# Optimization experiments

Hardware: AMD Instinct MI355X
Metric: run time of the kernel (lower is better)

## Reference

```python
import jax, jax.numpy as jnp
import numpy as np

BZ, SRC_LEN, TGT_LEN, DIM = 32, 1024, 1024, 512


def setup_inputs() -> dict:
    key = jax.random.key(0)
    k1, k2, k3, k4 = jax.random.split(key, 4)
    src = jax.random.normal(k1, (BZ, SRC_LEN, DIM), dtype=jnp.float32)
    tgt = jax.random.normal(k2, (BZ, TGT_LEN, DIM), dtype=jnp.float32)
    # lengths in [1, SRC_LEN] so every row has at least one valid position
    src_lengths = jax.random.randint(k3, (BZ,), 1, SRC_LEN + 1, dtype=jnp.int64)
    # nn.Linear(2*dim, dim, bias=False): weight shape (dim, 2*dim)
    bound = 1.0 / np.sqrt(2 * DIM)
    w_out = jax.random.uniform(k4, (DIM, 2 * DIM), dtype=jnp.float32,
                               minval=-bound, maxval=bound)
    return {"src": src, "tgt": tgt, "src_lengths": src_lengths, "w_out": w_out}


def reference(src, tgt, src_lengths, w_out):
    # dot-product attention scores: (bz, tgt_len, src_len)
    score = jnp.einsum("btd,bsd->bts", tgt, src)
    # mask out padded source positions (position >= length)
    valid = jnp.arange(src.shape[1])[None, :] < src_lengths[:, None]  # (bz, src_len)
    score = jnp.where(valid[:, None, :], score, -jnp.inf)
    align = jax.nn.softmax(score, axis=-1)
    # context: (bz, tgt_len, dim)
    c = jnp.einsum("bts,bsd->btd", align, src)
    concat_c = jnp.concatenate([c, tgt], axis=-1)  # (bz, tgt_len, 2*dim)
    attn_h = jnp.einsum("bte,de->btd", concat_c, w_out)
    return attn_h, align
```

## Files before the change

### kernel.cpp

```cpp
#include <hip/hip_runtime.h>
#include <hip/hip_bf16.h>

typedef __attribute__((ext_vector_type(4))) float  f32x4;
typedef __attribute__((ext_vector_type(4))) float  float4v;
typedef __attribute__((ext_vector_type(8))) short  bf16x8;
typedef __attribute__((ext_vector_type(4))) short  bf16x4;
typedef __attribute__((ext_vector_type(2))) unsigned int u32x2;

#define BZ   32
#define SLEN 1024
#define TLEN 1024
#define DIM  512
#define TILE 128
#define LP   40

#define PSEL 0x07060302u

__device__ __forceinline__ unsigned int fbits(float x) { return __builtin_bit_cast(unsigned int, x); }
__device__ __forceinline__ float fval(unsigned int u) { return __builtin_bit_cast(float, u); }

__device__ __forceinline__ unsigned short f2bf(float x) {
  unsigned int u = fbits(x);
  unsigned int r = u + 0x7FFFu + ((u >> 16) & 1u);
  return (unsigned short)(r >> 16);
}
__device__ __forceinline__ float bf2f(unsigned short h) { return fval(((unsigned int)h) << 16); }

__device__ __forceinline__ unsigned int packhi(float x0, float x1) {
  return __builtin_amdgcn_perm(fbits(x1), fbits(x0), PSEL);
}

__device__ __forceinline__ int get_len(const int* __restrict__ p, int b) {
  bool is64 = (p[1] == 0) && (p[3] == 0) && (p[5] == 0);
  return is64 ? p[2 * b] : p[b];
}

#define TLP 68
__global__ __launch_bounds__(256) void k_transpose(
    const float* __restrict__ src, unsigned short* __restrict__ srcT) {
  const int b  = blockIdx.z;
  const int s0 = blockIdx.x * 64;
  const int d0 = blockIdx.y * 64;
  __shared__ unsigned short tl[64 * TLP];
  const int tid = threadIdx.x;
#pragma unroll
  for (int r = 0; r < 4; ++r) {
    const int idx = tid + 256 * r;
    const int row = idx >> 4, c4 = idx & 15;
    float4v x = *(const float4v*)(src + ((size_t)(b * SLEN + s0 + row)) * DIM + d0 + c4 * 4);
    unsigned short* pp = tl + row * TLP + c4 * 4;
    pp[0] = f2bf(x[0]); pp[1] = f2bf(x[1]); pp[2] = f2bf(x[2]); pp[3] = f2bf(x[3]);
  }
  __syncthreads();
#pragma unroll
  for (int r = 0; r < 2; ++r) {
    const int idx  = tid + 256 * r;
    const int drow = idx >> 3, c8 = idx & 7;
    union { unsigned short u[8]; bf16x8 v; } pk;
#pragma unroll
    for (int j = 0; j < 8; ++j) pk.u[j] = tl[(c8 * 8 + j) * TLP + drow];
    *(bf16x8*)(srcT + ((size_t)(b * DIM + d0 + drow)) * SLEN + s0 + c8 * 8) = pk.v;
  }
}

__global__ __launch_bounds__(256) void k_prep_w(
    const float* __restrict__ w, unsigned short* __restrict__ wbf) {
  const size_t i = ((size_t)blockIdx.x * 256 + threadIdx.x) * 8;
  float4v x0 = *(const float4v*)(w + i);
  float4v x1 = *(const float4v*)(w + i + 4);
  union { unsigned short u[8]; bf16x8 v; } hi;
#pragma unroll
  for (int j = 0; j < 4; ++j) { hi.u[j] = f2bf(x0[j]); hi.u[4 + j] = f2bf(x1[j]); }
  *(bf16x8*)(wbf + i) = hi.v;
}

__global__ __launch_bounds__(256) void k_score(
    const float* __restrict__ tgt, const float* __restrict__ src,
    const int* __restrict__ lens, float* __restrict__ align_out) {
  const int j    = blockIdx.x;
  const int xcd  = j & 7;
  const int seq  = j >> 3;
  const int b    = ((seq >> 6) << 3) | xcd;
  const int tile = seq & 63;
  const int t0   = (tile >> 3) * TILE;
  const int s0   = (tile & 7) * TILE;
  const int len  = get_len(lens, b);
  if (s0 >= len) return;

  __shared__ short aHi[TILE * LP], aLo[TILE * LP], bHi[TILE * LP], bLo[TILE * LP];

  const int tid  = threadIdx.x;
  const int lane = tid & 63;
  const int wid  = tid >> 6;
  const int wt   = wid >> 1, wsd = wid & 1;
  const int g    = lane >> 4, r16 = lane & 15;
  const int srow = tid >> 3, sc4 = tid & 7;

  f32x4 acc[4][4];
#pragma unroll
  for (int m = 0; m < 4; ++m)
#pragma unroll
    for (int n = 0; n < 4; ++n) acc[m][n] = (f32x4){0.f, 0.f, 0.f, 0.f};

  const float* tgtB = tgt + ((size_t)(b * TLEN + t0)) * DIM;
  const float* srcB = src + ((size_t)(b * SLEN + s0)) * DIM;

  float4v va[4], vb[4];
#pragma unroll
  for (int r = 0; r < 4; ++r) {
    const int row = srow + 32 * r;
    va[r] = *(const float4v*)(tgtB + (size_t)row * DIM + sc4 * 4);
    vb[r] = *(const float4v*)(srcB + (size_t)row * DIM + sc4 * 4);
  }

  for (int k0 = 0; k0 < DIM; k0 += 32) {
#pragma unroll
    for (int r = 0; r < 4; ++r) {
      const int row = srow + 32 * r;
      u32x2 ah, al, bh, bl;
      ah[0] = packhi(va[r][0], va[r][1]); ah[1] = packhi(va[r][2], va[r][3]);
      bh[0] = packhi(vb[r][0], vb[r][1]); bh[1] = packhi(vb[r][2], vb[r][3]);
      float ra0 = va[r][0] - fval(fbits(va[r][0]) & 0xFFFF0000u);
      float ra1 = va[r][1] - fval(fbits(va[r][1]) & 0xFFFF0000u);
      float ra2 = va[r][2] - fval(fbits(va[r][2]) & 0xFFFF0000u);
      float ra3 = va[r][3] - fval(fbits(va[r][3]) & 0xFFFF0000u);
      float rb0 = vb[r][0] - fval(fbits(vb[r][0]) & 0xFFFF0000u);
      float rb1 = vb[r][1] - fval(fbits(vb[r][1]) & 0xFFFF0000u);
      float rb2 = vb[r][2] - fval(fbits(vb[r][2]) & 0xFFFF0000u);
      float rb3 = vb[r][3] - fval(fbits(vb[r][3]) & 0xFFFF0000u);
      al[0] = packhi(ra0, ra1); al[1] = packhi(ra2, ra3);
      bl[0] = packhi(rb0, rb1); bl[1] = packhi(rb2, rb3);
      const int o = row * LP + sc4 * 4;
      *(u32x2*)(aHi + o) = ah; *(u32x2*)(aLo + o) = al;
      *(u32x2*)(bHi + o) = bh; *(u32x2*)(bLo + o) = bl;
    }
    if (k0 + 32 < DIM) {
#pragma unroll
      for (int r = 0; r < 4; ++r) {
        const int row = srow + 32 * r;
        va[r] = *(const float4v*)(tgtB + (size_t)row * DIM + (k0 + 32) + sc4 * 4);
        vb[r] = *(const float4v*)(srcB + (size_t)row * DIM + (k0 + 32) + sc4 * 4);
      }
    }
    __syncthreads();
    bf16x8 fbh[4], fbl[4];
#pragma unroll
    for (int n = 0; n < 4; ++n) {
      const int row = wsd * 64 + n * 16 + r16;
      fbh[n] = *(const bf16x8*)(bHi + row * LP + g * 8);
      fbl[n] = *(const bf16x8*)(bLo + row * LP + g * 8);
    }
#pragma unroll
    for (int m = 0; m < 4; ++m) {
      const int row = wt * 64 + m * 16 + r16;
      bf16x8 fah = *(const bf16x8*)(aHi + row * LP + g * 8);
      bf16x8 fal = *(const bf16x8*)(aLo + row * LP + g * 8);
#pragma unroll
      for (int n = 0; n < 4; ++n) {
        acc[m][n] = __builtin_amdgcn_mfma_f32_16x16x32_bf16(fah, fbh[n], acc[m][n], 0, 0, 0);
        acc[m][n] = __builtin_amdgcn_mfma_f32_16x16x32_bf16(fal, fbh[n], acc[m][n], 0, 0, 0);
        acc[m][n] = __builtin_amdgcn_mfma_f32_16x16x32_bf16(fah, fbl[n], acc[m][n], 0, 0, 0);
      }
    }
    __syncthreads();
  }
  float* outB = align_out + ((size_t)(b * TLEN + t0)) * SLEN + s0;
#pragma unroll
  for (int m = 0; m < 4; ++m) {
    const int tr = wt * 64 + m * 16 + g * 4;
#pragma unroll
    for (int n = 0; n < 4; ++n) {
      const int sc = wsd * 64 + n * 16 + r16;
#pragma unroll
      for (int r = 0; r < 4; ++r)
        outB[(size_t)(tr + r) * SLEN + sc] = acc[m][n][r];
    }
  }
}

__global__ __launch_bounds__(256) void k_softmax(
    const int* __restrict__ lens, float* __restrict__ align_io) {
  const int row  = blockIdx.x * 4 + (threadIdx.x >> 6);
  const int lane = threadIdx.x & 63;
  const int b    = row >> 10;
  const int len  = get_len(lens, b);
  float* p = align_io + (size_t)row * SLEN;
  float v[4][4];
  float mx = -3.0e38f;
#pragma unroll
  for (int q = 0; q < 4; ++q) {
    if (256 * q >= len) {
#pragma unroll
      for (int j = 0; j < 4; ++j) v[q][j] = 0.f;
      continue;
    }
    const int sb = (lane + 64 * q) * 4;
    float4v x = *(const float4v*)(p + sb);
#pragma unroll
    for (int j = 0; j < 4; ++j) {
      v[q][j] = (sb + j < len) ? x[j] : 0.f;
      if (sb + j < len) mx = fmaxf(mx, x[j]);
    }
  }
#pragma unroll
  for (int off = 1; off < 64; off <<= 1) mx = fmaxf(mx, __shfl_xor(mx, off));
  float sum = 0.f;
#pragma unroll
  for (int q = 0; q < 4; ++q) {
    const int sb = (lane + 64 * q) * 4;
#pragma unroll
    for (int j = 0; j < 4; ++j) {
      float e = (sb + j < len) ? __expf(v[q][j] - mx) : 0.f;
      v[q][j] = e; sum += e;
    }
  }
#pragma unroll
  for (int off = 1; off < 64; off <<= 1) sum += __shfl_xor(sum, off);
  const float inv = 1.f / sum;
#pragma unroll
  for (int q = 0; q < 4; ++q) {
    float4v x;
#pragma unroll
    for (int j = 0; j < 4; ++j) x[j] = v[q][j] * inv;
    *(float4v*)(p + (lane + 64 * q) * 4) = x;
  }
}

__global__ __launch_bounds__(256) void k_pv(
    const float* __restrict__ align_in, const unsigned short* __restrict__ srcT,
    const int* __restrict__ lens, unsigned short* __restrict__ cws) {
  const int j    = blockIdx.x;
  const int xcd  = j & 7;
  const int seq  = j >> 3;
  const int b    = ((seq >> 5) << 3) | xcd;
  const int tile = seq & 31;
  const int t0   = (tile >> 2) * TILE;
  const int d0   = (tile & 3) * TILE;
  const int len = get_len(lens, b);
  const int ksteps = (len + 31) >> 5;

  __shared__ short A[TILE * LP], B[TILE * LP];
  const int tid  = threadIdx.x;
  const int lane = tid & 63;
  const int wid  = tid >> 6;
  const int wt   = wid >> 1, wsd = wid & 1;
  const int g    = lane >> 4, r16 = lane & 15;

  f32x4 acc[4][4];
#pragma unroll
  for (int m = 0; m < 4; ++m)
#pragma unroll
    for (int n = 0; n < 4; ++n) acc[m][n] = (f32x4){0.f, 0.f, 0.f, 0.f};

  const int arow = tid >> 3, ac4 = tid & 7;
  const int brow = tid >> 2, bc8 = tid & 3;

  float4v xa[4];
  bf16x8  xb[2];
#pragma unroll
  for (int r = 0; r < 4; ++r)
    xa[r] = *(const float4v*)(align_in + ((size_t)(b * TLEN + t0 + arow + 32 * r)) * SLEN + ac4 * 4);
#pragma unroll
  for (int r = 0; r < 2; ++r)
    xb[r] = *(const bf16x8*)(srcT + ((size_t)(b * DIM + d0 + brow + 64 * r)) * SLEN + bc8 * 8);

  for (int ks = 0; ks < ksteps; ++ks) {
#pragma unroll
    for (int r = 0; r < 4; ++r) {
      u32x2 h;
      h[0] = packhi(xa[r][0], xa[r][1]); h[1] = packhi(xa[r][2], xa[r][3]);
      *(u32x2*)(A + (arow + 32 * r) * LP + ac4 * 4) = h;
    }
#pragma unroll
    for (int r = 0; r < 2; ++r)
      *(bf16x8*)(B + (brow + 64 * r) * LP + bc8 * 8) = xb[r];
    if (ks + 1 < ksteps) {
      const int k0 = (ks + 1) * 32;
#pragma unroll
      for (int r = 0; r < 4; ++r)
        xa[r] = *(const float4v*)(align_in + ((size_t)(b * TLEN + t0 + arow + 32 * r)) * SLEN + k0 + ac4 * 4);
#pragma unroll
      for (int r = 0; r < 2; ++r)
        xb[r] = *(const bf16x8*)(srcT + ((size_t)(b * DIM + d0 + brow + 64 * r)) * SLEN + k0 + bc8 * 8);
    }
    __syncthreads();
    bf16x8 fb[4];
#pragma unroll
    for (int n = 0; n < 4; ++n) fb[n] = *(const bf16x8*)(B + (wsd * 64 + n * 16 + r16) * LP + g * 8);
#pragma unroll
    for (int m = 0; m < 4; ++m) {
      bf16x8 fa = *(const bf16x8*)(A + (wt * 64 + m * 16 + r16) * LP + g * 8);
#pragma unroll
      for (int n = 0; n < 4; ++n)
        acc[m][n] = __builtin_amdgcn_mfma_f32_16x16x32_bf16(fa, fb[n], acc[m][n], 0, 0, 0);
    }
    __syncthreads();
  }
#pragma unroll
  for (int m = 0; m < 4; ++m) {
    const int tr = wt * 64 + m * 16 + g * 4;
#pragma unroll
    for (int n = 0; n < 4; ++n) {
      const int dc = wsd * 64 + n * 16 + r16;
#pragma unroll
      for (int r = 0; r < 4; ++r)
        cws[((size_t)(b * TLEN + t0 + tr + r)) * DIM + d0 + dc] = f2bf(acc[m][n][r]);
    }
  }
}

__global__ __launch_bounds__(256) void k_proj(
    const unsigned short* __restrict__ cws, const float* __restrict__ tgt,
    const unsigned short* __restrict__ wbf, float* __restrict__ attn_out) {
  const int j    = blockIdx.x;
  const int xcd  = j & 7;
  const int seq  = j >> 3;
  const int b    = ((seq >> 5) << 3) | xcd;
  const int tile = seq & 31;
  const int t0   = (tile >> 2) * TILE;
  const int d0   = (tile & 3) * TILE;

  __shared__ short A[TILE * LP], B[TILE * LP];
  const int tid  = threadIdx.x;
  const int lane = tid & 63;
  const int wid  = tid >> 6;
  const int wt   = wid >> 1, wsd = wid & 1;
  const int g    = lane >> 4, r16 = lane & 15;

  f32x4 acc[4][4];
#pragma unroll
  for (int m = 0; m < 4; ++m)
#pragma unroll
    for (int n = 0; n < 4; ++n) acc[m][n] = (f32x4){0.f, 0.f, 0.f, 0.f};

  for (int k0 = 0; k0 < 2 * DIM; k0 += 32) {
    if (k0 < DIM) {
#pragma unroll
      for (int r = 0; r < 2; ++r) {
        const int row = (tid >> 2) + 64 * r, c8 = tid & 3;
        bf16x8 x = *(const bf16x8*)(cws + ((size_t)(b * TLEN + t0 + row)) * DIM + k0 + c8 * 8);
        *(bf16x8*)(A + row * LP + c8 * 8) = x;
      }
    } else {
#pragma unroll
      for (int r = 0; r < 4; ++r) {
        const int row = (tid >> 3) + 32 * r, c4 = tid & 7;
        float4v x = *(const float4v*)(tgt + ((size_t)(b * TLEN + t0 + row)) * DIM + (k0 - DIM) + c4 * 4);
        bf16x4 h;
#pragma unroll
        for (int j2 = 0; j2 < 4; ++j2) h[j2] = (short)f2bf(x[j2]);
        *(bf16x4*)(A + row * LP + c4 * 4) = h;
      }
    }
#pragma unroll
    for (int r = 0; r < 2; ++r) {
      const int row = (tid >> 2) + 64 * r, c8 = tid & 3;
      bf16x8 x = *(const bf16x8*)(wbf + ((size_t)(d0 + row)) * (2 * DIM) + k0 + c8 * 8);
      *(bf16x8*)(B + row * LP + c8 * 8) = x;
    }
    __syncthreads();
    bf16x8 fb[4];
#pragma unroll
    for (int n = 0; n < 4; ++n) fb[n] = *(const bf16x8*)(B + (wsd * 64 + n * 16 + r16) * LP + g * 8);
#pragma unroll
    for (int m = 0; m < 4; ++m) {
      bf16x8 fa = *(const bf16x8*)(A + (wt * 64 + m * 16 + r16) * LP + g * 8);
#pragma unroll
      for (int n = 0; n < 4; ++n)
        acc[m][n] = __builtin_amdgcn_mfma_f32_16x16x32_bf16(fa, fb[n], acc[m][n], 0, 0, 0);
    }
    __syncthreads();
  }
#pragma unroll
  for (int m = 0; m < 4; ++m) {
    const int tr = wt * 64 + m * 16 + g * 4;
#pragma unroll
    for (int n = 0; n < 4; ++n) {
      const int dc = wsd * 64 + n * 16 + r16;
#pragma unroll
      for (int r = 0; r < 4; ++r)
        attn_out[((size_t)(b * TLEN + t0 + tr + r)) * DIM + d0 + dc] = acc[m][n][r];
    }
  }
}

extern "C" void kernel_launch(void* const* d_in, const int* in_sizes, int n_in,
                              void* d_out, int out_size, void* d_ws, size_t ws_size,
                              hipStream_t stream) {
  const float* src   = (const float*)d_in[0];
  const float* tgt   = (const float*)d_in[1];
  const int*   lens  = (const int*)d_in[2];
  const float* w_out = (const float*)d_in[3];

  float* attn_out  = (float*)d_out;
  float* align_out = attn_out + (size_t)BZ * TLEN * DIM;

  const size_t NE = (size_t)BZ * SLEN * DIM;
  const size_t NW = (size_t)DIM * 2 * DIM;
  unsigned short* srcT = (unsigned short*)d_ws;
  unsigned short* cws  = srcT + NE;
  unsigned short* wbf  = cws + NE;

  k_transpose<<<dim3(16, 8, BZ), 256, 0, stream>>>(src, srcT);
  k_prep_w<<<dim3((unsigned)(NW / 8 / 256)), 256, 0, stream>>>(w_out, wbf);
  k_score<<<dim3(2048), 256, 0, stream>>>(tgt, src, lens, align_out);
  k_softmax<<<dim3(BZ * TLEN / 4), 256, 0, stream>>>(lens, align_out);
  k_pv<<<dim3(1024), 256, 0, stream>>>(align_out, srcT, lens, cws);
  k_proj<<<dim3(1024), 256, 0, stream>>>(cws, tgt, wbf, attn_out);
}
```

Measured before the change: 262.3 us.

## Precompute bf16 hi/lo splits and load score tiles via global_load_lds

The fp32-to-bf16 hi/lo split of src and tgt moves out of the score GEMM into prep kernels that write split copies to workspace. The score kernel then streams those copies straight into LDS with global_load_lds, without register staging or in-loop conversion. This removes the conversion ALU work and register pressure from the GEMM loop. In exchange it adds extra passes that write about four bf16 copies of the inputs, and it drops the LDS padding and the register prefetch of the next k-slice, which may cause bank conflicts and less overlap. The hi/lo split also changes from truncation to round-to-nearest.

Measured after the change: 300.2 us. +14.4%, slower.

```diff
diff --git a/kernel.cpp b/kernel.cpp
--- a/kernel.cpp
+++ b/kernel.cpp
@@ -30,26 +30,44 @@
   return __builtin_amdgcn_perm(fbits(x1), fbits(x0), PSEL);
 }
 
+__device__ __forceinline__ void gld16(const void* g, void* l) {
+  __builtin_amdgcn_global_load_lds(
+      (const __attribute__((address_space(1))) void*)g,
+      (__attribute__((address_space(3))) void*)l, 16, 0, 0);
+}
+
 __device__ __forceinline__ int get_len(const int* __restrict__ p, int b) {
   bool is64 = (p[1] == 0) && (p[3] == 0) && (p[5] == 0);
   return is64 ? p[2 * b] : p[b];
 }
 
 #define TLP 68
-__global__ __launch_bounds__(256) void k_transpose(
-    const float* __restrict__ src, unsigned short* __restrict__ srcT) {
+__global__ __launch_bounds__(256) void k_prep_src(
+    const float* __restrict__ src, unsigned short* __restrict__ srcT,
+    unsigned short* __restrict__ srcHi, unsigned short* __restrict__ srcLo) {
   const int b  = blockIdx.z;
   const int s0 = blockIdx.x * 64;
   const int d0 = blockIdx.y * 64;
   __shared__ unsigned short tl[64 * TLP];
   const int tid = threadIdx.x;
 #pragma unroll
-  for (int r = 0; r < 4; ++r) {
+  for (int r = 0; r < 2; ++r) {
     const int idx = tid + 256 * r;
-    const int row = idx >> 4, c4 = idx & 15;
-    float4v x = *(const float4v*)(src + ((size_t)(b * SLEN + s0 + row)) * DIM + d0 + c4 * 4);
-    unsigned short* pp = tl + row * TLP + c4 * 4;
-    pp[0] = f2bf(x[0]); pp[1] = f2bf(x[1]); pp[2] = f2bf(x[2]); pp[3] = f2bf(x[3]);
+    const int row = idx >> 3, c8 = idx & 7;
+    const size_t goff = ((size_t)(b * SLEN + s0 + row)) * DIM + d0 + c8 * 8;
+    float4v x0 = *(const float4v*)(src + goff);
+    float4v x1 = *(const float4v*)(src + goff + 4);
+    union { unsigned short u[8]; bf16x8 v; } hi, lo;
+#pragma unroll
+    for (int j = 0; j < 4; ++j) {
+      unsigned short h0 = f2bf(x0[j]);
+      hi.u[j] = h0; lo.u[j] = f2bf(x0[j] - bf2f(h0));
+      unsigned short h1 = f2bf(x1[j]);
+      hi.u[4 + j] = h1; lo.u[4 + j] = f2bf(x1[j] - bf2f(h1));
+    }
+    *(bf16x8*)(tl + row * TLP + c8 * 8) = hi.v;
+    *(bf16x8*)(srcHi + goff) = hi.v;
+    *(bf16x8*)(srcLo + goff) = lo.v;
   }
   __syncthreads();
 #pragma unroll
@@ -61,6 +79,24 @@
     for (int j = 0; j < 8; ++j) pk.u[j] = tl[(c8 * 8 + j) * TLP + drow];
     *(bf16x8*)(srcT + ((size_t)(b * DIM + d0 + drow)) * SLEN + s0 + c8 * 8) = pk.v;
   }
+}
+
+__global__ __launch_bounds__(256) void k_prep_tgt(
+    const float* __restrict__ tgt, unsigned short* __restrict__ hi_out,
+    unsigned short* __restrict__ lo_out) {
+  const size_t i = ((size_t)blockIdx.x * 256 + threadIdx.x) * 8;
+  float4v x0 = *(const float4v*)(tgt + i);
+  float4v x1 = *(const float4v*)(tgt + i + 4);
+  union { unsigned short u[8]; bf16x8 v; } hi, lo;
+#pragma unroll
+  for (int j = 0; j < 4; ++j) {
+    unsigned short h0 = f2bf(x0[j]);
+    hi.u[j] = h0; lo.u[j] = f2bf(x0[j] - bf2f(h0));
+    unsigned short h1 = f2bf(x1[j]);
+    hi.u[4 + j] = h1; lo.u[4 + j] = f2bf(x1[j] - bf2f(h1));
+  }
+  *(bf16x8*)(hi_out + i) = hi.v;
+  *(bf16x8*)(lo_out + i) = lo.v;
 }
 
 __global__ __launch_bounds__(256) void k_prep_w(
@@ -75,7 +111,8 @@
 }
 
 __global__ __launch_bounds__(256) void k_score(
-    const float* __restrict__ tgt, const float* __restrict__ src,
+    const unsigned short* __restrict__ tgtHi, const unsigned short* __restrict__ tgtLo,
+    const unsigned short* __restrict__ srcHi, const unsigned short* __restrict__ srcLo,
     const int* __restrict__ lens, float* __restrict__ align_out) {
   const int j    = blockIdx.x;
   const int xcd  = j & 7;
@@ -87,14 +124,27 @@
   const int len  = get_len(lens, b);
   if (s0 >= len) return;
 
-  __shared__ short aHi[TILE * LP], aLo[TILE * LP], bHi[TILE * LP], bLo[TILE * LP];
+  __shared__ short aHi[TILE * 32], aLo[TILE * 32], bHi[TILE * 32], bLo[TILE * 32];
 
   const int tid  = threadIdx.x;
   const int lane = tid & 63;
-  const int wid  = tid >> 6;
-  const int wt   = wid >> 1, wsd = wid & 1;
+  const int w    = tid >> 6;
+  const int wt   = w >> 1, wsd = w & 1;
   const int g    = lane >> 4, r16 = lane & 15;
-  const int srow = tid >> 3, sc4 = tid & 7;
+
+  const int rowA  = t0 + w * 32 + (lane >> 2);
+  const int rowB  = s0 + w * 32 + (lane >> 2);
+  const int c8    = (lane & 3) * 8;
+  const unsigned short* gAH = tgtHi + ((size_t)(b * TLEN + rowA)) * DIM + c8;
+  const unsigned short* gAL = tgtLo + ((size_t)(b * TLEN + rowA)) * DIM + c8;
+  const unsigned short* gBH = srcHi + ((size_t)(b * SLEN + rowB)) * DIM + c8;
+  const unsigned short* gBL = srcLo + ((size_t)(b * SLEN + rowB)) * DIM + c8;
+  const size_t rstep = (size_t)16 * DIM;
+
+  short* lAH = aHi + (w * 32) * 32;
+  short* lAL = aLo + (w * 32) * 32;
+  short* lBH = bHi + (w * 32) * 32;
+  short* lBL = bLo + (w * 32) * 32;
 
   f32x4 acc[4][4];
 #pragma unroll
@@ -102,59 +152,29 @@
 #pragma unroll
     for (int n = 0; n < 4; ++n) acc[m][n] = (f32x4){0.f, 0.f, 0.f, 0.f};
 
-  const float* tgtB = tgt + ((size_t)(b * TLEN + t0)) * DIM;
-  const float* srcB = src + ((size_t)(b * SLEN + s0)) * DIM;
-
-  float4v va[4], vb[4];
-#pragma unroll
-  for (int r = 0; r < 4; ++r) {
-    const int row = srow + 32 * r;
-    va[r] = *(const float4v*)(tgtB + (size_t)row * DIM + sc4 * 4);
-    vb[r] = *(const float4v*)(srcB + (size_t)row * DIM + sc4 * 4);
-  }
-
   for (int k0 = 0; k0 < DIM; k0 += 32) {
-#pragma unroll
-    for (int r = 0; r < 4; ++r) {
-      const int row = srow + 32 * r;
-      u32x2 ah, al, bh, bl;
-      ah[0] = packhi(va[r][0], va[r][1]); ah[1] = packhi(va[r][2], va[r][3]);
-      bh[0] = packhi(vb[r][0], vb[r][1]); bh[1] = packhi(vb[r][2], vb[r][3]);
-      float ra0 = va[r][0] - fval(fbits(va[r][0]) & 0xFFFF0000u);
-      float ra1 = va[r][1] - fval(fbits(va[r][1]) & 0xFFFF0000u);
-      float ra2 = va[r][2] - fval(fbits(va[r][2]) & 0xFFFF0000u);
-      float ra3 = va[r][3] - fval(fbits(va[r][3]) & 0xFFFF0000u);
-      float rb0 = vb[r][0] - fval(fbits(vb[r][0]) & 0xFFFF0000u);
-      float rb1 = vb[r][1] - fval(fbits(vb[r][1]) & 0xFFFF0000u);
-      float rb2 = vb[r][2] - fval(fbits(vb[r][2]) & 0xFFFF0000u);
-      float rb3 = vb[r][3] - fval(fbits(vb[r][3]) & 0xFFFF0000u);
-      al[0] = packhi(ra0, ra1); al[1] = packhi(ra2, ra3);
-      bl[0] = packhi(rb0, rb1); bl[1] = packhi(rb2, rb3);
-      const int o = row * LP + sc4 * 4;
-      *(u32x2*)(aHi + o) = ah; *(u32x2*)(aLo + o) = al;
-      *(u32x2*)(bHi + o) = bh; *(u32x2*)(bLo + o) = bl;
-    }
-    if (k0 + 32 < DIM) {
-#pragma unroll
-      for (int r = 0; r < 4; ++r) {
-        const int row = srow + 32 * r;
-        va[r] = *(const float4v*)(tgtB + (size_t)row * DIM + (k0 + 32) + sc4 * 4);
-        vb[r] = *(const float4v*)(srcB + (size_t)row * DIM + (k0 + 32) + sc4 * 4);
-      }
-    }
-    __syncthreads();
+    gld16(gAH + k0,         lAH);
+    gld16(gAH + k0 + rstep, lAH + 16 * 32);
+    gld16(gAL + k0,         lAL);
+    gld16(gAL + k0 + rstep, lAL + 16 * 32);
+    gld16(gBH + k0,         lBH);
+    gld16(gBH + k0 + rstep, lBH + 16 * 32);
+    gld16(gBL + k0,         lBL);
+    gld16(gBL + k0 + rstep, lBL + 16 * 32);
+    __syncthreads();
+
     bf16x8 fbh[4], fbl[4];
 #pragma unroll
     for (int n = 0; n < 4; ++n) {
       const int row = wsd * 64 + n * 16 + r16;
-      fbh[n] = *(const bf16x8*)(bHi + row * LP + g * 8);
-      fbl[n] = *(const bf16x8*)(bLo + row * LP + g * 8);
+      fbh[n] = *(const bf16x8*)(bHi + row * 32 + g * 8);
+      fbl[n] = *(const bf16x8*)(bLo + row * 32 + g * 8);
     }
 #pragma unroll
     for (int m = 0; m < 4; ++m) {
       const int row = wt * 64 + m * 16 + r16;
-      bf16x8 fah = *(const bf16x8*)(aHi + row * LP + g * 8);
-      bf16x8 fal = *(const bf16x8*)(aLo + row * LP + g * 8);
+      bf16x8 fah = *(const bf16x8*)(aHi + row * 32 + g * 8);
+      bf16x8 fal = *(const bf16x8*)(aLo + row * 32 + g * 8);
 #pragma unroll
       for (int n = 0; n < 4; ++n) {
         acc[m][n] = __builtin_amdgcn_mfma_f32_16x16x32_bf16(fah, fbh[n], acc[m][n], 0, 0, 0);
@@ -397,13 +417,18 @@
 
   const size_t NE = (size_t)BZ * SLEN * DIM;
   const size_t NW = (size_t)DIM * 2 * DIM;
-  unsigned short* srcT = (unsigned short*)d_ws;
-  unsigned short* cws  = srcT + NE;
-  unsigned short* wbf  = cws + NE;
-
-  k_transpose<<<dim3(16, 8, BZ), 256, 0, stream>>>(src, srcT);
+  unsigned short* srcT  = (unsigned short*)d_ws;
+  unsigned short* cws   = srcT + NE;
+  unsigned short* wbf   = cws + NE;
+  unsigned short* srcHi = wbf + NW;
+  unsigned short* srcLo = srcHi + NE;
+  unsigned short* tgtHi = srcLo + NE;
+  unsigned short* tgtLo = tgtHi + NE;
+
+  k_prep_src<<<dim3(16, 8, BZ), 256, 0, stream>>>(src, srcT, srcHi, srcLo);
+  k_prep_tgt<<<dim3((unsigned)(NE / 8 / 256)), 256, 0, stream>>>(tgt, tgtHi, tgtLo);
   k_prep_w<<<dim3((unsigned)(NW / 8 / 256)), 256, 0, stream>>>(w_out, wbf);
-  k_score<<<dim3(2048), 256, 0, stream>>>(tgt, src, lens, align_out);
+  k_score<<<dim3(2048), 256, 0, stream>>>(tgtHi, tgtLo, srcHi, srcLo, lens, align_out);
   k_softmax<<<dim3(BZ * TLEN / 4), 256, 0, stream>>>(lens, align_out);
   k_pv<<<dim3(1024), 256, 0, stream>>>(align_out, srcT, lens, cws);
   k_proj<<<dim3(1024), 256, 0, stream>>>(cws, tgt, wbf, attn_out);
```

## Fuse softmax normalization into PV kernel using precomputed row stats

Applied to the files above, without the earlier changes.

The softmax kernel now only computes each row's max and inverse sum and stores them as per-row stats, no longer writing the normalized row back. The PV kernel reads raw scores, applies exp and normalization on the fly while staging them to shared memory, and writes the final align output, with d-tiles splitting the writes round-robin and zero-filling masked tails. This removes one full write pass over the large score matrix, but the scores now go to a workspace buffer, and the four d-tiles each recompute the exponentials redundantly.

Measured after the change: 280.7 us. 7.0% more time.

```diff
diff --git a/kernel.cpp b/kernel.cpp
--- a/kernel.cpp
+++ b/kernel.cpp
@@ -76,7 +76,7 @@
 
 __global__ __launch_bounds__(256) void k_score(
     const float* __restrict__ tgt, const float* __restrict__ src,
-    const int* __restrict__ lens, float* __restrict__ align_out) {
+    const int* __restrict__ lens, float* __restrict__ raw_out) {
   const int j    = blockIdx.x;
   const int xcd  = j & 7;
   const int seq  = j >> 3;
@@ -164,7 +164,7 @@
     }
     __syncthreads();
   }
-  float* outB = align_out + ((size_t)(b * TLEN + t0)) * SLEN + s0;
+  float* outB = raw_out + ((size_t)(b * TLEN + t0)) * SLEN + s0;
 #pragma unroll
   for (int m = 0; m < 4; ++m) {
     const int tr = wt * 64 + m * 16 + g * 4;
@@ -178,13 +178,14 @@
   }
 }
 
-__global__ __launch_bounds__(256) void k_softmax(
-    const int* __restrict__ lens, float* __restrict__ align_io) {
+__global__ __launch_bounds__(256) void k_rowstat(
+    const int* __restrict__ lens, const float* __restrict__ raw,
+    float2* __restrict__ stats) {
   const int row  = blockIdx.x * 4 + (threadIdx.x >> 6);
   const int lane = threadIdx.x & 63;
   const int b    = row >> 10;
   const int len  = get_len(lens, b);
-  float* p = align_io + (size_t)row * SLEN;
+  const float* p = raw + (size_t)row * SLEN;
   float v[4][4];
   float mx = -3.0e38f;
 #pragma unroll
@@ -198,7 +199,7 @@
     float4v x = *(const float4v*)(p + sb);
 #pragma unroll
     for (int j = 0; j < 4; ++j) {
-      v[q][j] = (sb + j < len) ? x[j] : 0.f;
+      v[q][j] = x[j];
       if (sb + j < len) mx = fmaxf(mx, x[j]);
     }
   }
@@ -209,43 +210,42 @@
   for (int q = 0; q < 4; ++q) {
     const int sb = (lane + 64 * q) * 4;
 #pragma unroll
-    for (int j = 0; j < 4; ++j) {
-      float e = (sb + j < len) ? __expf(v[q][j] - mx) : 0.f;
-      v[q][j] = e; sum += e;
-    }
+    for (int j = 0; j < 4; ++j)
+      if (sb + j < len) sum += __expf(v[q][j] - mx);
   }
 #pragma unroll
   for (int off = 1; off < 64; off <<= 1) sum += __shfl_xor(sum, off);
-  const float inv = 1.f / sum;
-#pragma unroll
-  for (int q = 0; q < 4; ++q) {
-    float4v x;
-#pragma unroll
-    for (int j = 0; j < 4; ++j) x[j] = v[q][j] * inv;
-    *(float4v*)(p + (lane + 64 * q) * 4) = x;
-  }
+  if (lane == 0) stats[row] = make_float2(mx, 1.f / sum);
 }
 
 __global__ __launch_bounds__(256) void k_pv(
-    const float* __restrict__ align_in, const unsigned short* __restrict__ srcT,
-    const int* __restrict__ lens, unsigned short* __restrict__ cws) {
+    const float* __restrict__ raw, const unsigned short* __restrict__ srcT,
+    const int* __restrict__ lens, const float2* __restrict__ stats,
+    unsigned short* __restrict__ cws, float* __restrict__ align_out) {
   const int j    = blockIdx.x;
   const int xcd  = j & 7;
   const int seq  = j >> 3;
   const int b    = ((seq >> 5) << 3) | xcd;
   const int tile = seq & 31;
   const int t0   = (tile >> 2) * TILE;
-  const int d0   = (tile & 3) * TILE;
-  const int len = get_len(lens, b);
+  const int di   = tile & 3;
+  const int d0   = di * TILE;
+  const int len  = get_len(lens, b);
   const int ksteps = (len + 31) >> 5;
 
   __shared__ short A[TILE * LP], B[TILE * LP];
+  __shared__ float sM[TILE], sI[TILE];
   const int tid  = threadIdx.x;
   const int lane = tid & 63;
   const int wid  = tid >> 6;
   const int wt   = wid >> 1, wsd = wid & 1;
   const int g    = lane >> 4, r16 = lane & 15;
 
+  if (tid < TILE) {
+    float2 st = stats[b * TLEN + t0 + tid];
+    sM[tid] = st.x; sI[tid] = st.y;
+  }
+
   f32x4 acc[4][4];
 #pragma unroll
   for (int m = 0; m < 4; ++m)
@@ -259,17 +259,32 @@
   bf16x8  xb[2];
 #pragma unroll
   for (int r = 0; r < 4; ++r)
-    xa[r] = *(const float4v*)(align_in + ((size_t)(b * TLEN + t0 + arow + 32 * r)) * SLEN + ac4 * 4);
+    xa[r] = *(const float4v*)(raw + ((size_t)(b * TLEN + t0 + arow + 32 * r)) * SLEN + ac4 * 4);
 #pragma unroll
   for (int r = 0; r < 2; ++r)
     xb[r] = *(const bf16x8*)(srcT + ((size_t)(b * DIM + d0 + brow + 64 * r)) * SLEN + bc8 * 8);
 
+  __syncthreads();
+
   for (int ks = 0; ks < ksteps; ++ks) {
+    const bool wr = ((ks & 3) == di);
 #pragma unroll
     for (int r = 0; r < 4; ++r) {
+      const int row = arow + 32 * r;
+      const float m  = sM[row];
+      const float iv = sI[row];
+      const int sb = ks * 32 + ac4 * 4;
+      float4v p4;
+#pragma unroll
+      for (int jj = 0; jj < 4; ++jj) {
+        const int s = sb + jj;
+        p4[jj] = (s < len) ? __expf(xa[r][jj] - m) * iv : 0.f;
+      }
+      if (wr)
+        *(float4v*)(align_out + ((size_t)(b * TLEN + t0 + row)) * SLEN + sb) = p4;
       u32x2 h;
-      h[0] = packhi(xa[r][0], xa[r][1]); h[1] = packhi(xa[r][2], xa[r][3]);
-      *(u32x2*)(A + (arow + 32 * r) * LP + ac4 * 4) = h;
+      h[0] = packhi(p4[0], p4[1]); h[1] = packhi(p4[2], p4[3]);
+      *(u32x2*)(A + row * LP + ac4 * 4) = h;
     }
 #pragma unroll
     for (int r = 0; r < 2; ++r)
@@ -278,7 +293,7 @@
       const int k0 = (ks + 1) * 32;
 #pragma unroll
       for (int r = 0; r < 4; ++r)
-        xa[r] = *(const float4v*)(align_in + ((size_t)(b * TLEN + t0 + arow + 32 * r)) * SLEN + k0 + ac4 * 4);
+        xa[r] = *(const float4v*)(raw + ((size_t)(b * TLEN + t0 + arow + 32 * r)) * SLEN + k0 + ac4 * 4);
 #pragma unroll
       for (int r = 0; r < 2; ++r)
         xb[r] = *(const bf16x8*)(srcT + ((size_t)(b * DIM + d0 + brow + 64 * r)) * SLEN + k0 + bc8 * 8);
@@ -296,6 +311,18 @@
     }
     __syncthreads();
   }
+
+  {
+    const int ks_end = ksteps * 32;
+    const float4v z4 = {0.f, 0.f, 0.f, 0.f};
+    const int row = tid >> 3, c4 = tid & 7;
+    for (int s32 = ks_end + di * 32; s32 < SLEN; s32 += 128) {
+#pragma unroll
+      for (int r = 0; r < 4; ++r)
+        *(float4v*)(align_out + ((size_t)(b * TLEN + t0 + row + 32 * r)) * SLEN + s32 + c4 * 4) = z4;
+    }
+  }
+
 #pragma unroll
   for (int m = 0; m < 4; ++m) {
     const int tr = wt * 64 + m * 16 + g * 4;
@@ -397,14 +424,16 @@
 
   const size_t NE = (size_t)BZ * SLEN * DIM;
   const size_t NW = (size_t)DIM * 2 * DIM;
-  unsigned short* srcT = (unsigned short*)d_ws;
-  unsigned short* cws  = srcT + NE;
-  unsigned short* wbf  = cws + NE;
+  unsigned short* srcT  = (unsigned short*)d_ws;
+  unsigned short* cws   = srcT + NE;
+  unsigned short* wbf   = cws + NE;
+  float*          raw   = (float*)(wbf + NW);
+  float2*         stats = (float2*)(raw + (size_t)BZ * TLEN * SLEN);
 
   k_transpose<<<dim3(16, 8, BZ), 256, 0, stream>>>(src, srcT);
   k_prep_w<<<dim3((unsigned)(NW / 8 / 256)), 256, 0, stream>>>(w_out, wbf);
-  k_score<<<dim3(2048), 256, 0, stream>>>(tgt, src, lens, align_out);
-  k_softmax<<<dim3(BZ * TLEN / 4), 256, 0, stream>>>(lens, align_out);
-  k_pv<<<dim3(1024), 256, 0, stream>>>(align_out, srcT, lens, cws);
+  k_score<<<dim3(2048), 256, 0, stream>>>(tgt, src, lens, raw);
+  k_rowstat<<<dim3(BZ * TLEN / 4), 256, 0, stream>>>(lens, raw, stats);
+  k_pv<<<dim3(1024), 256, 0, stream>>>(raw, srcT, lens, stats, cws, align_out);
   k_proj<<<dim3(1024), 256, 0, stream>>>(cws, tgt, wbf, attn_out);
 }
```

## Emit bf16 probabilities from softmax and stream them into LDS directly in PV

Applied to the files above, without the earlier changes.

Softmax now also writes a bf16 copy of the probabilities to a new workspace buffer. The PV kernel reads that half-width copy instead of the fp32 align matrix, and uses global_load_lds to move A and B tiles straight from global memory into unpadded LDS. This drops the register round-trip, the in-kernel fp32-to-bf16 packing and the software prefetch. The cost is an extra 64MB write in softmax, loss of load/compute overlap in the K loop, and likely LDS bank conflicts from removing the row padding.

Measured after the change: 283.3 us. 1.08x slower.

```diff
diff --git a/kernel.cpp b/kernel.cpp
--- a/kernel.cpp
+++ b/kernel.cpp
@@ -28,6 +28,12 @@
 
 __device__ __forceinline__ unsigned int packhi(float x0, float x1) {
   return __builtin_amdgcn_perm(fbits(x1), fbits(x0), PSEL);
+}
+
+__device__ __forceinline__ void gld16(const void* g, void* l) {
+  __builtin_amdgcn_global_load_lds(
+      (const __attribute__((address_space(1))) void*)g,
+      (__attribute__((address_space(3))) void*)l, 16, 0, 0);
 }
 
 __device__ __forceinline__ int get_len(const int* __restrict__ p, int b) {
@@ -179,7 +185,8 @@
 }
 
 __global__ __launch_bounds__(256) void k_softmax(
-    const int* __restrict__ lens, float* __restrict__ align_io) {
+    const int* __restrict__ lens, float* __restrict__ align_io,
+    unsigned short* __restrict__ pbf) {
   const int row  = blockIdx.x * 4 + (threadIdx.x >> 6);
   const int lane = threadIdx.x & 63;
   const int b    = row >> 10;
@@ -217,17 +224,21 @@
 #pragma unroll
   for (int off = 1; off < 64; off <<= 1) sum += __shfl_xor(sum, off);
   const float inv = 1.f / sum;
+  unsigned short* pb = pbf + (size_t)row * SLEN;
 #pragma unroll
   for (int q = 0; q < 4; ++q) {
     float4v x;
 #pragma unroll
     for (int j = 0; j < 4; ++j) x[j] = v[q][j] * inv;
     *(float4v*)(p + (lane + 64 * q) * 4) = x;
+    u32x2 h;
+    h[0] = packhi(x[0], x[1]); h[1] = packhi(x[2], x[3]);
+    *(u32x2*)(pb + (lane + 64 * q) * 4) = h;
   }
 }
 
 __global__ __launch_bounds__(256) void k_pv(
-    const float* __restrict__ align_in, const unsigned short* __restrict__ srcT,
+    const unsigned short* __restrict__ pbf, const unsigned short* __restrict__ srcT,
     const int* __restrict__ lens, unsigned short* __restrict__ cws) {
   const int j    = blockIdx.x;
   const int xcd  = j & 7;
@@ -236,60 +247,44 @@
   const int tile = seq & 31;
   const int t0   = (tile >> 2) * TILE;
   const int d0   = (tile & 3) * TILE;
-  const int len = get_len(lens, b);
+  const int len  = get_len(lens, b);
   const int ksteps = (len + 31) >> 5;
 
-  __shared__ short A[TILE * LP], B[TILE * LP];
+  __shared__ short A[TILE * 32], B[TILE * 32];
+
   const int tid  = threadIdx.x;
   const int lane = tid & 63;
-  const int wid  = tid >> 6;
-  const int wt   = wid >> 1, wsd = wid & 1;
+  const int w    = tid >> 6;
+  const int wt   = w >> 1, wsd = w & 1;
   const int g    = lane >> 4, r16 = lane & 15;
 
+  const unsigned short* gA = pbf  + ((size_t)(b * TLEN + t0 + w * 32 + (lane >> 2))) * SLEN + (lane & 3) * 8;
+  const unsigned short* gB = srcT + ((size_t)(b * DIM  + d0 + w * 32 + (lane >> 2))) * SLEN + (lane & 3) * 8;
+  const size_t rstep = (size_t)16 * SLEN;
+  short* lA = A + (w * 32) * 32;
+  short* lB = B + (w * 32) * 32;
+
   f32x4 acc[4][4];
 #pragma unroll
   for (int m = 0; m < 4; ++m)
 #pragma unroll
     for (int n = 0; n < 4; ++n) acc[m][n] = (f32x4){0.f, 0.f, 0.f, 0.f};
 
-  const int arow = tid >> 3, ac4 = tid & 7;
-  const int brow = tid >> 2, bc8 = tid & 3;
-
-  float4v xa[4];
-  bf16x8  xb[2];
-#pragma unroll
-  for (int r = 0; r < 4; ++r)
-    xa[r] = *(const float4v*)(align_in + ((size_t)(b * TLEN + t0 + arow + 32 * r)) * SLEN + ac4 * 4);
-#pragma unroll
-  for (int r = 0; r < 2; ++r)
-    xb[r] = *(const bf16x8*)(srcT + ((size_t)(b * DIM + d0 + brow + 64 * r)) * SLEN + bc8 * 8);
-
   for (int ks = 0; ks < ksteps; ++ks) {
-#pragma unroll
-    for (int r = 0; r < 4; ++r) {
-      u32x2 h;
-      h[0] = packhi(xa[r][0], xa[r][1]); h[1] = packhi(xa[r][2], xa[r][3]);
-      *(u32x2*)(A + (arow + 32 * r) * LP + ac4 * 4) = h;
-    }
-#pragma unroll
-    for (int r = 0; r < 2; ++r)
-      *(bf16x8*)(B + (brow + 64 * r) * LP + bc8 * 8) = xb[r];
-    if (ks + 1 < ksteps) {
-      const int k0 = (ks + 1) * 32;
-#pragma unroll
-      for (int r = 0; r < 4; ++r)
-        xa[r] = *(const float4v*)(align_in + ((size_t)(b * TLEN + t0 + arow + 32 * r)) * SLEN + k0 + ac4 * 4);
-#pragma unroll
-      for (int r = 0; r < 2; ++r)
-        xb[r] = *(const bf16x8*)(srcT + ((size_t)(b * DIM + d0 + brow + 64 * r)) * SLEN + k0 + bc8 * 8);
-    }
-    __syncthreads();
+    const int k0 = ks * 32;
+    gld16(gA + k0,         lA);
+    gld16(gA + k0 + rstep, lA + 16 * 32);
+    gld16(gB + k0,         lB);
+    gld16(gB + k0 + rstep, lB + 16 * 32);
+    __syncthreads();
+
     bf16x8 fb[4];
 #pragma unroll
-    for (int n = 0; n < 4; ++n) fb[n] = *(const bf16x8*)(B + (wsd * 64 + n * 16 + r16) * LP + g * 8);
+    for (int n = 0; n < 4; ++n)
+      fb[n] = *(const bf16x8*)(B + (wsd * 64 + n * 16 + r16) * 32 + g * 8);
 #pragma unroll
     for (int m = 0; m < 4; ++m) {
-      bf16x8 fa = *(const bf16x8*)(A + (wt * 64 + m * 16 + r16) * LP + g * 8);
+      bf16x8 fa = *(const bf16x8*)(A + (wt * 64 + m * 16 + r16) * 32 + g * 8);
 #pragma unroll
       for (int n = 0; n < 4; ++n)
         acc[m][n] = __builtin_amdgcn_mfma_f32_16x16x32_bf16(fa, fb[n], acc[m][n], 0, 0, 0);
@@ -397,14 +392,16 @@
 
   const size_t NE = (size_t)BZ * SLEN * DIM;
   const size_t NW = (size_t)DIM * 2 * DIM;
+  const size_t NP = (size_t)BZ * TLEN * SLEN;
   unsigned short* srcT = (unsigned short*)d_ws;
   unsigned short* cws  = srcT + NE;
   unsigned short* wbf  = cws + NE;
+  unsigned short* pbf  = wbf + NW;
 
   k_transpose<<<dim3(16, 8, BZ), 256, 0, stream>>>(src, srcT);
   k_prep_w<<<dim3((unsigned)(NW / 8 / 256)), 256, 0, stream>>>(w_out, wbf);
   k_score<<<dim3(2048), 256, 0, stream>>>(tgt, src, lens, align_out);
-  k_softmax<<<dim3(BZ * TLEN / 4), 256, 0, stream>>>(lens, align_out);
-  k_pv<<<dim3(1024), 256, 0, stream>>>(align_out, srcT, lens, cws);
+  k_softmax<<<dim3(BZ * TLEN / 4), 256, 0, stream>>>(lens, align_out, pbf);
+  k_pv<<<dim3(1024), 256, 0, stream>>>(pbf, srcT, lens, cws);
   k_proj<<<dim3(1024), 256, 0, stream>>>(cws, tgt, wbf, attn_out);
 }
```
